# Optimization experiments

Hardware: AMD Instinct MI355X
Metric: run time of the kernel (lower is better)

## Reference

```python
import jax, jax.numpy as jnp
import numpy as np

D = 128
N1, N2, N3, N4 = 100000, 200000, 300000, 400000


def setup_inputs() -> dict:
    key = jax.random.key(0)
    cnt = [0]

    def nrm(shape, scale=0.05):
        cnt[0] += 1
        return jax.random.normal(jax.random.fold_in(key, cnt[0]), shape, dtype=jnp.float32) * scale

    def rint(shape, hi):
        cnt[0] += 1
        return jax.random.randint(jax.random.fold_in(key, cnt[0]), shape, 0, hi)

    inp = {}
    inp["h"] = nrm((N1, D), 1.0)
    inp["idx2"] = rint((N2, 2), N1)
    inp["idx3"] = rint((N3, 3), N1)
    inp["idx4"] = rint((N4, 4), N1)
    # sequential_%L MLPs: Linear(L*D -> D) + relu, Linear(D->D)+relu, Linear(D->D)+relu
    for L in (1, 2, 3, 4):
        din = D * L
        inp["s%d_W0" % L] = nrm((din, D))
        inp["s%d_b0" % L] = nrm((D,))
        inp["s%d_W1" % L] = nrm((D, D))
        inp["s%d_b1" % L] = nrm((D,))
        inp["s%d_W2" % L] = nrm((D, D))
        inp["s%d_b2" % L] = nrm((D,))
    # per-feature output heads Linear(D -> 1)
    for f in ("sigma", "epsilon", "q"):
        inp["h1_%s_W" % f] = nrm((D, 1))
        inp["h1_%s_b" % f] = nrm((1,))
    for L in (2, 3, 4):
        for f in ("k", "eq"):
            inp["h%d_%s_W" % (L, f)] = nrm((D, 1))
            inp["h%d_%s_b" % (L, f)] = nrm((1,))
    return inp


def _mlp(x, W0, b0, W1, b1, W2, b2):
    x = jax.nn.relu(x @ W0 + b0)
    x = jax.nn.relu(x @ W1 + b1)
    return jax.nn.relu(x @ W2 + b2)


def _level(h, idx, p):
    # copy_u + mean with exactly one n1 neighbor per relationship slot == gather
    g = jnp.take(h, idx, axis=0)              # [N, K, D]
    N, K, Dd = g.shape
    xf = g.reshape(N, K * Dd)                 # concat h0..h_{K-1}
    xb = g[:, ::-1, :].reshape(N, K * Dd)     # concat reversed
    return _mlp(xf, *p) + _mlp(xb, *p)        # pool = torch.add


def reference(h, idx2, idx3, idx4,
              s1_W0, s1_b0, s1_W1, s1_b1, s1_W2, s1_b2,
              s2_W0, s2_b0, s2_W1, s2_b1, s2_W2, s2_b2,
              s3_W0, s3_b0, s3_W1, s3_b1, s3_W2, s3_b2,
              s4_W0, s4_b0, s4_W1, s4_b1, s4_W2, s4_b2,
              h1_sigma_W, h1_sigma_b, h1_epsilon_W, h1_epsilon_b, h1_q_W, h1_q_b,
              h2_k_W, h2_k_b, h2_eq_W, h2_eq_b,
              h3_k_W, h3_k_b, h3_eq_W, h3_eq_b,
              h4_k_W, h4_k_b, h4_eq_W, h4_eq_b):
    y1 = _mlp(h, s1_W0, s1_b0, s1_W1, s1_b1, s1_W2, s1_b2)
    sigma = y1 @ h1_sigma_W + h1_sigma_b
    epsilon = y1 @ h1_epsilon_W + h1_epsilon_b
    q = y1 @ h1_q_W + h1_q_b
    y2 = _level(h, idx2, (s2_W0, s2_b0, s2_W1, s2_b1, s2_W2, s2_b2))
    k2 = y2 @ h2_k_W + h2_k_b
    eq2 = y2 @ h2_eq_W + h2_eq_b
    y3 = _level(h, idx3, (s3_W0, s3_b0, s3_W1, s3_b1, s3_W2, s3_b2))
    k3 = y3 @ h3_k_W + h3_k_b
    eq3 = y3 @ h3_eq_W + h3_eq_b
    y4 = _level(h, idx4, (s4_W0, s4_b0, s4_W1, s4_b1, s4_W2, s4_b2))
    k4 = y4 @ h4_k_W + h4_k_b
    eq4 = y4 @ h4_eq_W + h4_eq_b
    return (sigma, epsilon, q, k2, eq2, k3, eq3, k4, eq4)
```

## Files before the change

### kernel.cpp

```cpp
#include <hip/hip_runtime.h>

typedef __attribute__((ext_vector_type(8))) _Float16 half8;
typedef __attribute__((ext_vector_type(4))) float f32x4;

#define N1_ 100000
#define N2_ 200000
#define N3_ 300000
#define N4_ 400000

typedef __attribute__((address_space(1))) const void gconst_t;
typedef __attribute__((address_space(3))) void lds_t;

__device__ __forceinline__ unsigned short f2h_bits(float x) {
  union { _Float16 h; unsigned short u; } cv;
  cv.h = (_Float16)x;
  return cv.u;
}

__device__ __forceinline__ f32x4 mfma16(half8 a, half8 b, f32x4 c) {
  return __builtin_amdgcn_mfma_f32_16x16x32_f16(a, b, c, 0, 0, 0);
}

__global__ void cvt_h_kernel(const float* __restrict__ h,
                             unsigned short* __restrict__ hf, int n4) {
  int i = blockIdx.x * blockDim.x + threadIdx.x;
  if (i >= n4) return;
  float4 v = reinterpret_cast<const float4*>(h)[i];
  ushort4 o;
  o.x = f2h_bits(v.x); o.y = f2h_bits(v.y);
  o.z = f2h_bits(v.z); o.w = f2h_bits(v.w);
  reinterpret_cast<ushort4*>(hf)[i] = o;
}

struct PackInfo {
  const float* W[12];
  int kt_base[13];
  int out_off[12];
};

__global__ void pack_w_kernel(PackInfo info, unsigned short* __restrict__ pw) {
  int b = blockIdx.x;
  int lane = threadIdx.x;
  int m = 0;
  while (m < 11 && b >= info.kt_base[m + 1]) ++m;
  int kt = b - info.kt_base[m];
  const float* W = info.W[m];
  int lr = lane & 15, kb = lane >> 4;
  unsigned short* outp = pw + info.out_off[m] + (size_t)kt * 4096 + lane * 8;
  #pragma unroll
  for (int nt = 0; nt < 8; ++nt) {
    #pragma unroll
    for (int j = 0; j < 8; ++j) {
      int krow = kt * 32 + kb * 8 + j;
      int col = nt * 16 + lr;
      outp[nt * 512 + j] = f2h_bits(W[(size_t)krow * 128 + col]);
    }
  }
}

template <int K, int NHEAD>
__global__ __launch_bounds__(256, 2) void level_kernel(
    const unsigned short* __restrict__ hf,
    const int* __restrict__ idx,
    const unsigned short* __restrict__ pw,
    const float* __restrict__ b0, const float* __restrict__ b1,
    const float* __restrict__ b2,
    const float* __restrict__ hw0, const float* __restrict__ hb0,
    float* __restrict__ out0,
    const float* __restrict__ hw1, const float* __restrict__ hb1,
    float* __restrict__ out1,
    const float* __restrict__ hw2, const float* __restrict__ hb2,
    float* __restrict__ out2,
    int N) {
  constexpr int NDIR = (K > 1) ? 2 : 1;
  constexpr int KT0 = 4 * K;

  __shared__ __align__(16) unsigned short bstage[2][4096];
  __shared__ __align__(16) unsigned short act[4][NDIR][2][2048];

  const int lane = threadIdx.x & 63;
  const int wid = threadIdx.x >> 6;
  const int lrow = lane & 15;
  const int kb = lane >> 4;

  const int wtile = (blockIdx.x * 4 + wid) * 2;
  const int maxtile = N / 16 - 1;
  int tile[2];
  bool wr[2];
  #pragma unroll
  for (int t = 0; t < 2; ++t) {
    wr[t] = (wtile + t <= maxtile);
    tile[t] = wr[t] ? (wtile + t) : maxtile;
  }

  int src[2][K];
  #pragma unroll
  for (int t = 0; t < 2; ++t)
    #pragma unroll
    for (int s = 0; s < K; ++s)
      src[t][s] = (K == 1) ? (tile[t] * 16 + lrow)
                           : idx[(size_t)(tile[t] * 16 + lrow) * K + s];

  auto stage = [&](int buf, const unsigned short* slab) {
    const unsigned short* g = slab + (wid * 2) * 512 + lane * 8;
    unsigned short* l = &bstage[buf][(wid * 2) * 512];
    __builtin_amdgcn_global_load_lds((gconst_t*)g, (lds_t*)l, 16, 0, 0);
    __builtin_amdgcn_global_load_lds((gconst_t*)(g + 512), (lds_t*)(l + 512), 16, 0, 0);
  };

  auto gload = [&](int kt, half8 (*f)[NDIR]) {
    int seg = kt >> 2, sub = kt & 3;
    #pragma unroll
    for (int t = 0; t < 2; ++t) {
      f[t][0] = *reinterpret_cast<const half8*>(
          hf + (size_t)src[t][seg] * 128 + sub * 32 + kb * 8);
      if constexpr (NDIR == 2)
        f[t][1] = *reinterpret_cast<const half8*>(
            hf + (size_t)src[t][K - 1 - seg] * 128 + sub * 32 + kb * 8);
    }
  };

  auto actA = [&](int t, int d, int kt) -> half8 {
    unsigned off = (unsigned)(lrow * 256 + (kt * 32 + kb * 8) * 2) ^
                   ((unsigned)(lrow & 7) << 4);
    return *reinterpret_cast<const half8*>(
        reinterpret_cast<const unsigned char*>(&act[wid][d][t][0]) + off);
  };

  f32x4 acc[2][NDIR][8];
  auto zero_acc = [&]() {
    #pragma unroll
    for (int t = 0; t < 2; ++t)
      #pragma unroll
      for (int d = 0; d < NDIR; ++d)
        #pragma unroll
        for (int nt = 0; nt < 8; ++nt) acc[t][d][nt] = f32x4{0.f, 0.f, 0.f, 0.f};
  };

  auto store_act = [&](int t, int d, const float* bias) {
    unsigned char* base = reinterpret_cast<unsigned char*>(&act[wid][d][t][0]);
    #pragma unroll
    for (int nt = 0; nt < 8; ++nt) {
      float bv = bias[nt * 16 + lrow];
      #pragma unroll
      for (int r = 0; r < 4; ++r) {
        float v = fmaxf(acc[t][d][nt][r] + bv, 0.f);
        int trow = 4 * kb + r;
        unsigned off = (unsigned)(trow * 256 + (nt * 16 + lrow) * 2) ^
                       ((unsigned)(trow & 7) << 4);
        *reinterpret_cast<unsigned short*>(base + off) = f2h_bits(v);
      }
    }
  };

  int cur = 0;

  zero_acc();
  half8 aCur[2][NDIR], aNxt[2][NDIR];
  stage(cur, pw);
  gload(0, aCur);
  __syncthreads();
  for (int kt = 0; kt < KT0; ++kt) {
    if (kt + 1 < KT0) {
      stage(cur ^ 1, pw + (size_t)(kt + 1) * 4096);
      gload(kt + 1, aNxt);
    }
    #pragma unroll
    for (int nt = 0; nt < 8; ++nt) {
      half8 bq = *reinterpret_cast<const half8*>(&bstage[cur][nt * 512 + lane * 8]);
      #pragma unroll
      for (int t = 0; t < 2; ++t)
        #pragma unroll
        for (int d = 0; d < NDIR; ++d)
          acc[t][d][nt] = mfma16(aCur[t][d], bq, acc[t][d][nt]);
    }
    __syncthreads();
    cur ^= 1;
    #pragma unroll
    for (int t = 0; t < 2; ++t)
      #pragma unroll
      for (int d = 0; d < NDIR; ++d) aCur[t][d] = aNxt[t][d];
  }
  #pragma unroll
  for (int t = 0; t < 2; ++t)
    #pragma unroll
    for (int d = 0; d < NDIR; ++d) store_act(t, d, b0);

  const unsigned short* wptr[2] = {pw + (size_t)KT0 * 4096,
                                   pw + (size_t)KT0 * 4096 + 16384};
  #pragma unroll 1
  for (int layer = 1; layer <= 2; ++layer) {
    const unsigned short* w = wptr[layer - 1];
    zero_acc();
    stage(cur, w);
    __syncthreads();
    for (int kt = 0; kt < 4; ++kt) {
      if (kt + 1 < 4) stage(cur ^ 1, w + (size_t)(kt + 1) * 4096);
      half8 a[2][NDIR];
      #pragma unroll
      for (int t = 0; t < 2; ++t)
        #pragma unroll
        for (int d = 0; d < NDIR; ++d) a[t][d] = actA(t, d, kt);
      #pragma unroll
      for (int nt = 0; nt < 8; ++nt) {
        half8 bq = *reinterpret_cast<const half8*>(&bstage[cur][nt * 512 + lane * 8]);
        #pragma unroll
        for (int t = 0; t < 2; ++t)
          #pragma unroll
          for (int d = 0; d < NDIR; ++d)
            acc[t][d][nt] = mfma16(a[t][d], bq, acc[t][d][nt]);
      }
      __syncthreads();
      cur ^= 1;
    }
    if (layer == 1) {
      #pragma unroll
      for (int t = 0; t < 2; ++t)
        #pragma unroll
        for (int d = 0; d < NDIR; ++d) store_act(t, d, b1);
    }
  }

  const float* hws[3] = {hw0, hw1, hw2};
  const float* hbs[3] = {hb0, hb1, hb2};
  float* outs[3] = {out0, out1, out2};

  #pragma unroll
  for (int t = 0; t < 2; ++t) {
    f32x4 y[8];
    #pragma unroll
    for (int nt = 0; nt < 8; ++nt) {
      float bv = b2[nt * 16 + lrow];
      #pragma unroll
      for (int r = 0; r < 4; ++r) {
        float v = fmaxf(acc[t][0][nt][r] + bv, 0.f);
        if constexpr (NDIR == 2) v += fmaxf(acc[t][1][nt][r] + bv, 0.f);
        y[nt][r] = v;
      }
    }
    #pragma unroll
    for (int hd = 0; hd < NHEAD; ++hd) {
      float p[4] = {0.f, 0.f, 0.f, 0.f};
      #pragma unroll
      for (int nt = 0; nt < 8; ++nt) {
        float w = hws[hd][nt * 16 + lrow];
        #pragma unroll
        for (int r = 0; r < 4; ++r) p[r] += y[nt][r] * w;
      }
      #pragma unroll
      for (int m = 1; m < 16; m <<= 1) {
        #pragma unroll
        for (int r = 0; r < 4; ++r) p[r] += __shfl_xor(p[r], m, 64);
      }
      if (wr[t] && lrow < 4) {
        float pv = (lrow == 0) ? p[0] : (lrow == 1) ? p[1] : (lrow == 2) ? p[2] : p[3];
        outs[hd][tile[t] * 16 + 4 * kb + lrow] = pv + hbs[hd][0];
      }
    }
  }
}

extern "C" void kernel_launch(void* const* d_in, const int* in_sizes, int n_in,
                              void* d_out, int out_size, void* d_ws, size_t ws_size,
                              hipStream_t stream) {
  (void)in_sizes; (void)n_in; (void)out_size;

  const float* h = (const float*)d_in[0];
  const int* idx2 = (const int*)d_in[1];
  const int* idx3 = (const int*)d_in[2];
  const int* idx4 = (const int*)d_in[3];

  const float* sW[4][3];
  const float* sb[4][3];
  for (int L = 0; L < 4; ++L)
    for (int j = 0; j < 3; ++j) {
      sW[L][j] = (const float*)d_in[4 + L * 6 + j * 2];
      sb[L][j] = (const float*)d_in[4 + L * 6 + j * 2 + 1];
    }
  const float* hW[9];
  const float* hB[9];
  for (int i = 0; i < 9; ++i) {
    hW[i] = (const float*)d_in[28 + i * 2];
    hB[i] = (const float*)d_in[28 + i * 2 + 1];
  }

  size_t need = ((size_t)N1_ * 128 + 294912) * 2;
  if (ws_size < need) return;
  unsigned short* hf = (unsigned short*)d_ws;
  unsigned short* pw = hf + (size_t)N1_ * 128;

  cvt_h_kernel<<<(N1_ * 128 / 4 + 255) / 256, 256, 0, stream>>>(h, hf, N1_ * 128 / 4);

  PackInfo pi;
  const int din[12] = {128, 128, 128, 256, 128, 128, 384, 128, 128, 512, 128, 128};
  int ktb = 0, ooff = 0;
  for (int m = 0; m < 12; ++m) {
    pi.W[m] = sW[m / 3][m % 3];
    pi.kt_base[m] = ktb;
    pi.out_off[m] = ooff;
    ktb += din[m] / 32;
    ooff += din[m] * 128;
  }
  pi.kt_base[12] = ktb;
  pack_w_kernel<<<ktb, 64, 0, stream>>>(pi, pw);

  float* out = (float*)d_out;
  float* o_sigma = out;
  float* o_eps = out + N1_;
  float* o_q = out + 2 * N1_;
  float* o_k2 = out + 3 * N1_;
  float* o_eq2 = o_k2 + N2_;
  float* o_k3 = o_eq2 + N2_;
  float* o_eq3 = o_k3 + N3_;
  float* o_k4 = o_eq3 + N3_;
  float* o_eq4 = o_k4 + N4_;

  level_kernel<1, 3><<<(N1_ / 16 + 7) / 8, 256, 0, stream>>>(
      hf, nullptr, pw + pi.out_off[0], sb[0][0], sb[0][1], sb[0][2],
      hW[0], hB[0], o_sigma, hW[1], hB[1], o_eps, hW[2], hB[2], o_q, N1_);
  level_kernel<2, 2><<<(N2_ / 16 + 7) / 8, 256, 0, stream>>>(
      hf, idx2, pw + pi.out_off[3], sb[1][0], sb[1][1], sb[1][2],
      hW[3], hB[3], o_k2, hW[4], hB[4], o_eq2, nullptr, nullptr, nullptr, N2_);
  level_kernel<3, 2><<<(N3_ / 16 + 7) / 8, 256, 0, stream>>>(
      hf, idx3, pw + pi.out_off[6], sb[2][0], sb[2][1], sb[2][2],
      hW[5], hB[5], o_k3, hW[6], hB[6], o_eq3, nullptr, nullptr, nullptr, N3_);
  level_kernel<4, 2><<<(N4_ / 16 + 7) / 8, 256, 0, stream>>>(
      hf, idx4, pw + pi.out_off[9], sb[3][0], sb[3][1], sb[3][2],
      hW[7], hB[7], o_k4, hW[8], hB[8], o_eq4, nullptr, nullptr, nullptr, N4_);
}
```

Measured before the change: 522.4 us.

## Pair mirrored weight slabs to reuse gathered rows for both directions

Layer 0 now walks weight slabs in mirrored pairs (segment s, then segment K-1-s). One gathered fragment of h then feeds both the forward and the reversed MLP accumulators, so each neighbor row is fetched from global memory once instead of twice. Odd K handles the middle segment in a separate loop. The first slab of the next layer is also prefetched during the previous layer, which drops the prologue barriers between layers. In exchange the control flow is more intricate and the slab order changes.

```diff
diff --git a/kernel.cpp b/kernel.cpp
--- a/kernel.cpp
+++ b/kernel.cpp
@@ -74,6 +74,8 @@
     int N) {
   constexpr int NDIR = (K > 1) ? 2 : 1;
   constexpr int KT0 = 4 * K;
+  constexpr int NPAIR = (K / 2) * 4;
+  constexpr bool MID = (K % 2) != 0;
 
   __shared__ __align__(16) unsigned short bstage[2][4096];
   __shared__ __align__(16) unsigned short act[4][NDIR][2][2048];
@@ -108,15 +110,32 @@
     __builtin_amdgcn_global_load_lds((gconst_t*)(g + 512), (lds_t*)(l + 512), 16, 0, 0);
   };
 
-  auto gload = [&](int kt, half8 (*f)[NDIR]) {
-    int seg = kt >> 2, sub = kt & 3;
-    #pragma unroll
-    for (int t = 0; t < 2; ++t) {
-      f[t][0] = *reinterpret_cast<const half8*>(
-          hf + (size_t)src[t][seg] * 128 + sub * 32 + kb * 8);
-      if constexpr (NDIR == 2)
-        f[t][1] = *reinterpret_cast<const half8*>(
-            hf + (size_t)src[t][K - 1 - seg] * 128 + sub * 32 + kb * 8);
+  auto gfrag = [&](int segRow, int sub, half8* dst) {
+    #pragma unroll
+    for (int t = 0; t < 2; ++t)
+      dst[t] = *reinterpret_cast<const half8*>(
+          hf + (size_t)src[t][segRow] * 128 + sub * 32 + kb * 8);
+  };
+
+  f32x4 acc[2][NDIR][8];
+  auto zero_acc = [&]() {
+    #pragma unroll
+    for (int t = 0; t < 2; ++t)
+      #pragma unroll
+      for (int d = 0; d < NDIR; ++d)
+        #pragma unroll
+        for (int nt = 0; nt < 8; ++nt) acc[t][d][nt] = f32x4{0.f, 0.f, 0.f, 0.f};
+  };
+
+  auto mfma_phase = [&](int buf, half8* af, half8* ab) {
+    #pragma unroll
+    for (int nt = 0; nt < 8; ++nt) {
+      half8 bq = *reinterpret_cast<const half8*>(&bstage[buf][nt * 512 + lane * 8]);
+      #pragma unroll
+      for (int t = 0; t < 2; ++t) {
+        acc[t][0][nt] = mfma16(af[t], bq, acc[t][0][nt]);
+        if constexpr (NDIR == 2) acc[t][1][nt] = mfma16(ab[t], bq, acc[t][1][nt]);
+      }
     }
   };
 
@@ -125,16 +144,6 @@
                    ((unsigned)(lrow & 7) << 4);
     return *reinterpret_cast<const half8*>(
         reinterpret_cast<const unsigned char*>(&act[wid][d][t][0]) + off);
-  };
-
-  f32x4 acc[2][NDIR][8];
-  auto zero_acc = [&]() {
-    #pragma unroll
-    for (int t = 0; t < 2; ++t)
-      #pragma unroll
-      for (int d = 0; d < NDIR; ++d)
-        #pragma unroll
-        for (int nt = 0; nt < 8; ++nt) acc[t][d][nt] = f32x4{0.f, 0.f, 0.f, 0.f};
   };
 
   auto store_act = [&](int t, int d, const float* bias) {
@@ -154,48 +163,69 @@
   };
 
   int cur = 0;
-
   zero_acc();
-  half8 aCur[2][NDIR], aNxt[2][NDIR];
+
+  half8 gA[2], gB[2], nA[2], nB[2];
   stage(cur, pw);
-  gload(0, aCur);
+  gfrag(0, 0, gA);
+  if constexpr (NPAIR > 0) gfrag(K - 1, 0, gB);
   __syncthreads();
-  for (int kt = 0; kt < KT0; ++kt) {
-    if (kt + 1 < KT0) {
-      stage(cur ^ 1, pw + (size_t)(kt + 1) * 4096);
-      gload(kt + 1, aNxt);
-    }
-    #pragma unroll
-    for (int nt = 0; nt < 8; ++nt) {
-      half8 bq = *reinterpret_cast<const half8*>(&bstage[cur][nt * 512 + lane * 8]);
-      #pragma unroll
-      for (int t = 0; t < 2; ++t)
-        #pragma unroll
-        for (int d = 0; d < NDIR; ++d)
-          acc[t][d][nt] = mfma16(aCur[t][d], bq, acc[t][d][nt]);
-    }
+
+  for (int pr = 0; pr < NPAIR; ++pr) {
+    const int sp = pr >> 2, sub = pr & 3;
+    const int slabB = (K - 1 - sp) * 4 + sub;
+    stage(cur ^ 1, pw + (size_t)slabB * 4096);
+    mfma_phase(cur, gA, gB);
     __syncthreads();
     cur ^= 1;
-    #pragma unroll
-    for (int t = 0; t < 2; ++t)
-      #pragma unroll
-      for (int d = 0; d < NDIR; ++d) aCur[t][d] = aNxt[t][d];
-  }
+    if (pr + 1 < NPAIR) {
+      const int sp2 = (pr + 1) >> 2, sub2 = (pr + 1) & 3;
+      stage(cur ^ 1, pw + (size_t)(sp2 * 4 + sub2) * 4096);
+      gfrag(sp2, sub2, nA);
+      gfrag(K - 1 - sp2, sub2, nB);
+    } else if constexpr (MID) {
+      stage(cur ^ 1, pw + (size_t)(((K - 1) / 2) * 4) * 4096);
+      gfrag((K - 1) / 2, 0, nA);
+    } else {
+      stage(cur ^ 1, pw + (size_t)KT0 * 4096);
+    }
+    mfma_phase(cur, gB, gA);
+    __syncthreads();
+    cur ^= 1;
+    #pragma unroll
+    for (int t = 0; t < 2; ++t) { gA[t] = nA[t]; gB[t] = nB[t]; }
+  }
+
+  if constexpr (MID) {
+    const int mseg = (K - 1) / 2;
+    for (int sub = 0; sub < 4; ++sub) {
+      if (sub + 1 < 4) {
+        stage(cur ^ 1, pw + (size_t)(mseg * 4 + sub + 1) * 4096);
+        gfrag(mseg, sub + 1, nA);
+      } else {
+        stage(cur ^ 1, pw + (size_t)KT0 * 4096);
+      }
+      mfma_phase(cur, gA, gA);
+      __syncthreads();
+      cur ^= 1;
+      #pragma unroll
+      for (int t = 0; t < 2; ++t) gA[t] = nA[t];
+    }
+  }
+
   #pragma unroll
   for (int t = 0; t < 2; ++t)
     #pragma unroll
     for (int d = 0; d < NDIR; ++d) store_act(t, d, b0);
 
-  const unsigned short* wptr[2] = {pw + (size_t)KT0 * 4096,
-                                   pw + (size_t)KT0 * 4096 + 16384};
+  const unsigned short* w1 = pw + (size_t)KT0 * 4096;
   #pragma unroll 1
   for (int layer = 1; layer <= 2; ++layer) {
-    const unsigned short* w = wptr[layer - 1];
+    const unsigned short* w = (layer == 1) ? w1 : w1 + 16384;
     zero_acc();
-    stage(cur, w);
-    __syncthreads();
     for (int kt = 0; kt < 4; ++kt) {
       if (kt + 1 < 4) stage(cur ^ 1, w + (size_t)(kt + 1) * 4096);
+      else if (layer == 1) stage(cur ^ 1, w1 + 16384);
       half8 a[2][NDIR];
       #pragma unroll
       for (int t = 0; t < 2; ++t)
@@ -210,8 +240,10 @@
           for (int d = 0; d < NDIR; ++d)
             acc[t][d][nt] = mfma16(a[t][d], bq, acc[t][d][nt]);
       }
-      __syncthreads();
-      cur ^= 1;
+      if (!(layer == 2 && kt == 3)) {
+        __syncthreads();
+        cur ^= 1;
+      }
     }
     if (layer == 1) {
       #pragma unroll
```

Measured after the change: 449.5 us. 14.0% less time.
